# Optimization experiments

Hardware: AMD Instinct MI355X
Metric: run time of the kernel (lower is better)

The kernel has to match this reference:

```python
import jax, jax.numpy as jnp
import numpy as np

N_NODES = 50000
N_EDGES = 400000
LATENT = 128
HIDDEN = 512
N_HEADS = 2          # latent // 64, NodeAttn default num_heads
HEAD_DIM = LATENT // N_HEADS
N_GRAPHS = 500
LN_EPS = 1e-5


def setup_inputs() -> dict:
    key = jax.random.key(0)
    ks = jax.random.split(key, 24)
    s = 0.02
    inp = {
        "edges": jax.random.randint(ks[0], (2, N_EDGES), 0, N_NODES, dtype=jnp.int32),
        "node_feat": jax.random.normal(ks[1], (N_NODES, LATENT), jnp.float32),
        "edge_attr": jax.random.normal(ks[2], (N_EDGES, LATENT), jnp.float32),
        "u": jax.random.normal(ks[3], (N_GRAPHS, LATENT), jnp.float32),
        "num_nodes": jnp.full((N_GRAPHS,), N_NODES // N_GRAPHS, jnp.int32),
        # NodeAttn params (shared for sent/received calls, as in the module)
        "w1": jax.random.normal(ks[4], (3 * LATENT, LATENT), jnp.float32) * s,
        "b1": jnp.zeros((LATENT,), jnp.float32),
        "w2": jax.random.normal(ks[5], (N_HEADS, HEAD_DIM), jnp.float32) * s,
        "w3": jax.random.normal(ks[6], (2 * LATENT, LATENT), jnp.float32) * s,
        "b3": jnp.zeros((LATENT,), jnp.float32),
        # Encoder MLP: 4*latent -> hidden -> hidden -> latent, LN before ReLU
        "mw0": jax.random.normal(ks[7], (4 * LATENT, HIDDEN), jnp.float32) * s,
        "mb0": jnp.zeros((HIDDEN,), jnp.float32),
        "ls0": jnp.ones((HIDDEN,), jnp.float32),
        "lb0": jnp.zeros((HIDDEN,), jnp.float32),
        "mw1": jax.random.normal(ks[8], (HIDDEN, HIDDEN), jnp.float32) * s,
        "mb1": jnp.zeros((HIDDEN,), jnp.float32),
        "ls1": jnp.ones((HIDDEN,), jnp.float32),
        "lb1": jnp.zeros((HIDDEN,), jnp.float32),
        "mw2": jax.random.normal(ks[9], (HIDDEN, LATENT), jnp.float32) * s,
        "mb2": jnp.zeros((LATENT,), jnp.float32),
    }
    return inp


def _layer_norm(x, scale, bias):
    mu = jnp.mean(x, axis=-1, keepdims=True)
    var = jnp.mean(jnp.square(x - mu), axis=-1, keepdims=True)
    return (x - mu) * jax.lax.rsqrt(var + LN_EPS) * scale + bias


def _node_attn(q, k, ea, index, n_nodes, w1, b1, w2, w3, b3):
    # per-edge multi-head scores -> segment softmax over destination index -> scatter-add
    h = jax.nn.leaky_relu(jnp.concatenate([q, k, ea], axis=-1) @ w1 + b1, 0.2)
    h = h.reshape(-1, N_HEADS, HEAD_DIM)                    # [E, H, D]
    logits = jnp.einsum("ehd,hd->eh", h, w2)                 # [E, H]
    m = jax.ops.segment_max(logits, index, num_segments=n_nodes)
    m = jnp.where(jnp.isfinite(m), m, 0.0)                   # empty segments
    e = jnp.exp(logits - m[index])
    z = jax.ops.segment_sum(e, index, num_segments=n_nodes)
    alpha = e / (z[index] + 1e-16)                           # [E, H]
    v = (jnp.concatenate([k, ea], axis=-1) @ w3 + b3).reshape(-1, N_HEADS, HEAD_DIM)
    out = jax.ops.segment_sum(alpha[..., None] * v, index, num_segments=n_nodes)
    return out.reshape(n_nodes, LATENT)


def reference(edges, node_feat, edge_attr, u, num_nodes, w1, b1, w2, w3, b3,
              mw0, mb0, ls0, lb0, mw1, mb1, ls1, lb1, mw2, mb2):
    n = node_feat.shape[0]
    row, col = edges[0], edges[1]
    sent = _node_attn(node_feat[row], node_feat[col], edge_attr, row, n, w1, b1, w2, w3, b3)
    recv = _node_attn(node_feat[col], node_feat[row], edge_attr, col, n, w1, b1, w2, w3, b3)
    glob = jnp.repeat(u, num_nodes, axis=0, total_repeat_length=n)
    x = jnp.concatenate([node_feat, sent, recv, glob], axis=1)   # [N, 4*latent]
    h = jax.nn.relu(_layer_norm(x @ mw0 + mb0, ls0, lb0))
    h = jax.nn.relu(_layer_norm(h @ mw1 + mb1, ls1, lb1))
    return h @ mw2 + mb2
```

## Files before the change

### kernel.cpp

```cpp
#include <hip/hip_runtime.h>
#include <math.h>

#define LATENT 128

typedef __attribute__((ext_vector_type(8))) short bf16x8;
typedef __attribute__((ext_vector_type(4))) float f32x4;
typedef __attribute__((ext_vector_type(2))) float f32x2;
typedef __attribute__((ext_vector_type(2))) unsigned u32x2;
typedef __attribute__((ext_vector_type(4))) unsigned u32x4;

union U4B { uint4 u; bf16x8 v; };

template <typename T>
__device__ __forceinline__ T ntl(const T* p) { return __builtin_nontemporal_load(p); }

__device__ __forceinline__ unsigned short f2bf(float f) {
    unsigned int x = __float_as_uint(f);
    unsigned int r = (x + 0x7fffu + ((x >> 16) & 1u)) >> 16;
    return (unsigned short)r;
}
__device__ __forceinline__ float bf2f(unsigned short h) {
    return __uint_as_float(((unsigned int)h) << 16);
}
__device__ __forceinline__ unsigned pk2(float a, float b) {
    return (unsigned)f2bf(a) | ((unsigned)f2bf(b) << 16);
}
__device__ __forceinline__ float lo16(unsigned u) { return __uint_as_float(u << 16); }
__device__ __forceinline__ float hi16(unsigned u) { return __uint_as_float(u & 0xffff0000u); }

__device__ __forceinline__ void gld16(const void* g, void* l) {
    __builtin_amdgcn_global_load_lds(
        (const __attribute__((address_space(1))) unsigned int*)g,
        (__attribute__((address_space(3))) unsigned int*)l, 16, 0, 0);
}

__global__ void k_gidfill(const int* __restrict__ goff, int G, int n, int* __restrict__ gid) {
    int i = blockIdx.x * 256 + threadIdx.x;
    if (i >= n) return;
    int lo = 0, hi = G - 1;
    while (lo < hi) {
        int mid = (lo + hi + 1) >> 1;
        if (goff[mid] <= i) lo = mid; else hi = mid - 1;
    }
    gid[i] = lo;
}

#define FN  1152
#define FE3 1248
#define FEV 1280
__global__ __launch_bounds__(256) void k_pack2(const float* __restrict__ mw0,
                                               const float* __restrict__ mw1,
                                               const float* __restrict__ mw2,
                                               const float* __restrict__ w1,
                                               const float* __restrict__ w3,
                                               uint4* __restrict__ pw) {
    int tid = blockIdx.x * 256 + threadIdx.x;
    if (tid >= 1312 * 64) return;
    int fid = tid >> 6, lane = tid & 63;
    const float* src; int kt, nt, N;
    if (fid < 512)       { src = mw0;            kt = fid >> 5;           nt = fid & 31;           N = 512; }
    else if (fid < 1024) { src = mw1;            kt = (fid - 512) >> 5;   nt = (fid - 512) & 31;   N = 512; }
    else if (fid < 1152) { src = mw2;            kt = (fid - 1024) >> 3;  nt = (fid - 1024) & 7;   N = 128; }
    else if (fid < 1184) { src = w1;             kt = (fid - 1152) >> 3;  nt = (fid - 1152) & 7;   N = 128; }
    else if (fid < 1216) { src = w1 + 128 * 128; kt = (fid - 1184) >> 3;  nt = (fid - 1184) & 7;   N = 128; }
    else if (fid < 1248) { src = w3;             kt = (fid - 1216) >> 3;  nt = (fid - 1216) & 7;   N = 128; }
    else if (fid < 1280) { src = w1 + 256 * 128; kt = (fid - 1248) >> 3;  nt = (fid - 1248) & 7;   N = 128; }
    else                 { src = w3 + 128 * 128; kt = (fid - 1280) >> 3;  nt = (fid - 1280) & 7;   N = 128; }
    int col = nt * 16 + (lane & 15);
    int k0 = kt * 32 + (lane >> 4) * 8;
    unsigned int w[4];
#pragma unroll
    for (int p = 0; p < 4; ++p) {
        unsigned int lo = f2bf(src[(size_t)(k0 + 2 * p) * N + col]);
        unsigned int hi = f2bf(src[(size_t)(k0 + 2 * p + 1) * N + col]);
        w[p] = lo | (hi << 16);
    }
    pw[(size_t)fid * 64 + lane] = make_uint4(w[0], w[1], w[2], w[3]);
}

__global__ void k_count(const int* __restrict__ edges, int E,
                        int* __restrict__ deg_s, int* __restrict__ deg_r) {
    int e = blockIdx.x * 256 + threadIdx.x;
    if (e < E) { atomicAdd(&deg_s[edges[e]], 1); atomicAdd(&deg_r[edges[E + e]], 1); }
}

__global__ __launch_bounds__(1024) void k_scan(const int* __restrict__ deg, int n,
                                               int* __restrict__ rowptr, int* __restrict__ cursor) {
    __shared__ int wsum[16];
    int t = threadIdx.x;
    int chunk = (n + 1023) / 1024;
    int s = t * chunk; if (s > n) s = n;
    int epos = s + chunk; if (epos > n) epos = n;
    int sum = 0;
    for (int i = s; i < epos; ++i) sum += deg[i];
    int lane = t & 63, wid = t >> 6;
    int v = sum;
#pragma unroll
    for (int d = 1; d < 64; d <<= 1) { int o = __shfl_up(v, d); if (lane >= d) v += o; }
    if (lane == 63) wsum[wid] = v;
    __syncthreads();
    if (t < 16) {
        int wv = wsum[t];
#pragma unroll
        for (int d = 1; d < 16; d <<= 1) { int o = __shfl_up(wv, d, 16); if (t >= d) wv += o; }
        wsum[t] = wv;
    }
    __syncthreads();
    int woff = wid ? wsum[wid - 1] : 0;
    int run = v + woff - sum;
    for (int i = s; i < epos; ++i) { rowptr[i] = run; if (cursor) cursor[i] = run; run += deg[i]; }
    if (t == 1023) rowptr[n] = run;
}

__global__ void k_fill(const int* __restrict__ edges, int E,
                       int* __restrict__ cur_s, int* __restrict__ cur_r,
                       int* __restrict__ sm_s, int* __restrict__ sm_r) {
    int e = blockIdx.x * 256 + threadIdx.x;
    if (e < E) {
        int r = edges[e], c = edges[E + e];
        sm_s[e] = atomicAdd(&cur_s[r], 1);
        sm_r[e] = atomicAdd(&cur_r[c], 1);
    }
}

__global__ __launch_bounds__(512) void k_nodepre2(const float* __restrict__ nf, int n,
                                                  const uint4* __restrict__ pw,
                                                  unsigned short* __restrict__ PQK,
                                                  unsigned short* __restrict__ PVh) {
    __shared__ uint4 xs[32 * 64];
    int t = threadIdx.x, lane = t & 63, w = t >> 6;
    int wr = w >> 2, wc = w & 3, l15 = lane & 15, lg = lane >> 4;
    int base = blockIdx.x * 128;
#pragma unroll
    for (int it = 0; it < 4; ++it) {
        int chunk = t + it * 512;
        int row = chunk >> 4, k8 = chunk & 15, k = k8 * 8;
        int node = base + row;
        f32x4 v0 = (f32x4)(0.f), v1 = (f32x4)(0.f);
        if (node < n) {
            const f32x4* s4 = (const f32x4*)(nf + (size_t)node * 128 + k);
            v0 = ntl(s4); v1 = ntl(s4 + 1);
        }
        uint4 pkv;
        pkv.x = pk2(v0.x, v0.y); pkv.y = pk2(v0.z, v0.w);
        pkv.z = pk2(v1.x, v1.y); pkv.w = pk2(v1.z, v1.w);
        int kt = k >> 5, g = (k >> 3) & 3;
        xs[(kt * 8 + (row >> 4)) * 64 + g * 16 + (row & 15)] = pkv;
    }
    __syncthreads();
    f32x4 acc[4][6];
#pragma unroll
    for (int rt = 0; rt < 4; ++rt)
#pragma unroll
        for (int ct = 0; ct < 6; ++ct) acc[rt][ct] = (f32x4)(0.f);
    for (int kt = 0; kt < 4; ++kt) {
        U4B a[4];
#pragma unroll
        for (int rt = 0; rt < 4; ++rt) a[rt].u = xs[(kt * 8 + wr * 4 + rt) * 64 + lane];
        U4B b[6];
#pragma unroll
        for (int ct = 0; ct < 6; ++ct) {
            int nt = wc * 6 + ct;
            int mat = nt >> 3, ntm = nt & 7;
            b[ct].u = pw[(size_t)(FN + mat * 32 + kt * 8 + ntm) * 64 + lane];
        }
#pragma unroll
        for (int rt = 0; rt < 4; ++rt)
#pragma unroll
            for (int ct = 0; ct < 6; ++ct)
                acc[rt][ct] = __builtin_amdgcn_mfma_f32_16x16x32_bf16(a[rt].v, b[ct].v, acc[rt][ct], 0, 0, 0);
    }
#pragma unroll
    for (int rt = 0; rt < 4; ++rt)
#pragma unroll
        for (int ct = 0; ct < 6; ++ct) {
            int nt = wc * 6 + ct;
#pragma unroll
            for (int reg = 0; reg < 4; ++reg) {
                int node = base + (wr * 4 + rt) * 16 + lg * 4 + reg;
                if (node < n) {
                    unsigned short hv = f2bf(acc[rt][ct][reg]);
                    if (nt < 16) PQK[(size_t)node * 256 + nt * 16 + l15] = hv;
                    else         PVh[(size_t)node * 128 + (nt - 16) * 16 + l15] = hv;
                }
            }
        }
}

__global__ __launch_bounds__(256) void k_eproj1(const int* __restrict__ edges,
                                                const float* __restrict__ ea, int E,
                                                const uint4* __restrict__ pw,
                                                const unsigned short* __restrict__ PQK,
                                                const unsigned short* __restrict__ PVh,
                                                const float* __restrict__ b1,
                                                const float* __restrict__ w2,
                                                const float* __restrict__ b3,
                                                const int* __restrict__ sm_s,
                                                const int* __restrict__ sm_r,
                                                unsigned short* __restrict__ Vs,
                                                unsigned short* __restrict__ Vr,
                                                float* __restrict__ ess2, float* __restrict__ ers2) {
    __shared__ char lds[49152];
    uint4* xs = (uint4*)lds;
    char* ldsE = lds + 16384;
    char* ldsV = lds + 32768;
    int t = threadIdx.x, lane = t & 63, w = t >> 6;
    int wc = w, l15 = lane & 15, lg = lane >> 4;
    int base = blockIdx.x * 64;
#pragma unroll
    for (int it = 0; it < 4; ++it) {
        int chunk = t + it * 256;
        int row = chunk >> 4, k8 = chunk & 15, k = k8 * 8;
        int e = base + row;
        f32x4 v0 = (f32x4)(0.f), v1 = (f32x4)(0.f);
        if (e < E) {
            const f32x4* s4 = (const f32x4*)(ea + (size_t)e * 128 + k);
            v0 = ntl(s4); v1 = ntl(s4 + 1);
        }
        uint4 pkv;
        pkv.x = pk2(v0.x, v0.y); pkv.y = pk2(v0.z, v0.w);
        pkv.z = pk2(v1.x, v1.y); pkv.w = pk2(v1.z, v1.w);
        int kt = k >> 5, g = (k >> 3) & 3;
        xs[(kt * 4 + (row >> 4)) * 64 + g * 16 + (row & 15)] = pkv;
    }
    __syncthreads();
#pragma unroll
    for (int pass = 0; pass < 2; ++pass) {
        f32x4 acc[2][4];
#pragma unroll
        for (int rt2 = 0; rt2 < 2; ++rt2)
#pragma unroll
            for (int ct = 0; ct < 4; ++ct) acc[rt2][ct] = (f32x4)(0.f);
        for (int kt = 0; kt < 4; ++kt) {
            U4B a[2];
#pragma unroll
            for (int rt2 = 0; rt2 < 2; ++rt2)
                a[rt2].u = xs[(kt * 4 + pass * 2 + rt2) * 64 + lane];
            U4B b[4];
            b[0].u = pw[(size_t)(FE3 + kt * 8 + wc * 2 + 0) * 64 + lane];
            b[1].u = pw[(size_t)(FE3 + kt * 8 + wc * 2 + 1) * 64 + lane];
            b[2].u = pw[(size_t)(FEV + kt * 8 + wc * 2 + 0) * 64 + lane];
            b[3].u = pw[(size_t)(FEV + kt * 8 + wc * 2 + 1) * 64 + lane];
#pragma unroll
            for (int rt2 = 0; rt2 < 2; ++rt2)
#pragma unroll
                for (int ct = 0; ct < 4; ++ct)
                    acc[rt2][ct] = __builtin_amdgcn_mfma_f32_16x16x32_bf16(a[rt2].v, b[ct].v, acc[rt2][ct], 0, 0, 0);
        }
#pragma unroll
        for (int rt2 = 0; rt2 < 2; ++rt2)
#pragma unroll
            for (int cc = 0; cc < 2; ++cc) {
                int col = (wc * 2 + cc) * 16 + l15;
                float b1c = b1[col], b3c = b3[col];
#pragma unroll
                for (int reg = 0; reg < 4; ++reg) {
                    int e_loc = (pass * 2 + rt2) * 16 + lg * 4 + reg;
                    int off = (e_loc * 256 + col * 2) ^ ((e_loc & 7) << 4);
                    *(unsigned short*)(ldsE + off) = f2bf(acc[rt2][cc][reg] + b1c);
                    *(unsigned short*)(ldsV + off) = f2bf(acc[rt2][2 + cc][reg] + b3c);
                }
            }
    }
    __syncthreads();
    {
        int e4 = lane >> 4, piece = lane & 15;
#pragma unroll
        for (int i = 0; i < 4; ++i) {
            int e_loc = w * 16 + i * 4 + e4;
            int e = base + e_loc;
            if (e < E) {
                int r = edges[e], c = edges[E + e];
                int off = (e_loc * 256 + piece * 16) ^ ((e_loc & 7) << 4);
                u32x4 vev = *(const u32x4*)(ldsV + off);
                u32x4 pvc = *(const u32x4*)(PVh + (size_t)c * 128 + piece * 8);
                u32x4 pvr = *(const u32x4*)(PVh + (size_t)r * 128 + piece * 8);
                u32x4 vs, vr;
#pragma unroll
                for (int q = 0; q < 4; ++q) {
                    float e0 = lo16(vev[q]);
                    float e1 = hi16(vev[q]);
                    vs[q] = pk2(e0 + lo16(pvc[q]), e1 + hi16(pvc[q]));
                    vr[q] = pk2(e0 + lo16(pvr[q]), e1 + hi16(pvr[q]));
                }
                __builtin_nontemporal_store(vs, (u32x4*)(Vs + (size_t)sm_s[e] * 128 + piece * 8));
                __builtin_nontemporal_store(vr, (u32x4*)(Vr + (size_t)sm_r[e] * 128 + piece * 8));
            }
        }
    }
    int esub = lane >> 3, dg = lane & 7;
    float w2r[16];
    {
        const float4* w4 = (const float4*)(w2 + (dg >> 2) * 64 + (dg & 3) * 16);
#pragma unroll
        for (int q = 0; q < 4; ++q) {
            float4 wv = w4[q];
            w2r[q * 4 + 0] = wv.x; w2r[q * 4 + 1] = wv.y; w2r[q * 4 + 2] = wv.z; w2r[q * 4 + 3] = wv.w;
        }
    }
#pragma unroll
    for (int it = 0; it < 2; ++it) {
        int e_loc = w * 16 + it * 8 + esub;
        int e = base + e_loc;
        if (e >= E) break;
        int r = edges[e], c = edges[E + e];
        const uint4* Aqr = (const uint4*)(PQK + ((size_t)r << 8) + dg * 16);
        const uint4* Akc = (const uint4*)(PQK + ((size_t)c << 8) + 128 + dg * 16);
        const uint4* Aqc = (const uint4*)(PQK + ((size_t)c << 8) + dg * 16);
        const uint4* Akr = (const uint4*)(PQK + ((size_t)r << 8) + 128 + dg * 16);
        float ps = 0.f, pr = 0.f;
#pragma unroll
        for (int half = 0; half < 2; ++half) {
            int off3 = (e_loc * 256 + dg * 32 + half * 16) ^ ((e_loc & 7) << 4);
            uint4 ue3 = *(const uint4*)(ldsE + off3);
            uint4 uqr = Aqr[half], ukc = Akc[half], uqc = Aqc[half], ukr = Akr[half];
            unsigned wqr[4] = {uqr.x, uqr.y, uqr.z, uqr.w};
            unsigned wkc[4] = {ukc.x, ukc.y, ukc.z, ukc.w};
            unsigned wqc[4] = {uqc.x, uqc.y, uqc.z, uqc.w};
            unsigned wkr[4] = {ukr.x, ukr.y, ukr.z, ukr.w};
            unsigned we3[4] = {ue3.x, ue3.y, ue3.z, ue3.w};
#pragma unroll
            for (int q = 0; q < 4; ++q) {
#pragma unroll
                for (int hl = 0; hl < 2; ++hl) {
                    int i = half * 8 + q * 2 + hl;
                    float fqr = hl ? hi16(wqr[q]) : lo16(wqr[q]);
                    float fkc = hl ? hi16(wkc[q]) : lo16(wkc[q]);
                    float fqc = hl ? hi16(wqc[q]) : lo16(wqc[q]);
                    float fkr = hl ? hi16(wkr[q]) : lo16(wkr[q]);
                    float com = hl ? hi16(we3[q]) : lo16(we3[q]);
                    float hs = fqr + fkc + com; hs = hs > 0.f ? hs : 0.2f * hs;
                    float hr = fqc + fkr + com; hr = hr > 0.f ? hr : 0.2f * hr;
                    ps += hs * w2r[i]; pr += hr * w2r[i];
                }
            }
        }
        ps += __shfl_xor(ps, 1); ps += __shfl_xor(ps, 2);
        pr += __shfl_xor(pr, 1); pr += __shfl_xor(pr, 2);
        float Es = expf(ps), Er = expf(pr);
        if (dg == 0) {
            __builtin_nontemporal_store(Es, &ess2[(size_t)sm_s[e] * 2]);
            __builtin_nontemporal_store(Er, &ers2[(size_t)sm_r[e] * 2]);
        } else if (dg == 4) {
            __builtin_nontemporal_store(Es, &ess2[(size_t)sm_s[e] * 2 + 1]);
            __builtin_nontemporal_store(Er, &ers2[(size_t)sm_r[e] * 2 + 1]);
        }
    }
}

__global__ __launch_bounds__(256) void k_aggr(int n,
                                              const int* __restrict__ rps, const int* __restrict__ rpr,
                                              const float* __restrict__ ess2, const float* __restrict__ ers2,
                                              const unsigned short* __restrict__ Vs,
                                              const unsigned short* __restrict__ Vr,
                                              unsigned short* __restrict__ out_sh,
                                              unsigned short* __restrict__ out_rh) {
    int w = threadIdx.x >> 6, lane = threadIdx.x & 63;
    int unit = blockIdx.x * 4 + w;
    if (unit >= 2 * n) return;
    bool sent = unit < n;
    int node = sent ? unit : unit - n;
    const int*      rp = sent ? rps : rpr;
    const float*    ex = sent ? ess2 : ers2;
    const unsigned* V  = (const unsigned*)(sent ? Vs : Vr);
    int s0 = rp[node], s1 = rp[node + 1];
    float z0 = 0.f, z1 = 0.f, acca = 0.f, accb = 0.f;
    int j = s0;
    for (; j + 4 <= s1; j += 4) {
        f32x2 ez[4]; unsigned v[4];
#pragma unroll
        for (int q = 0; q < 4; ++q) ez[q] = ntl((const f32x2*)(ex + 2 * (j + q)));
#pragma unroll
        for (int q = 0; q < 4; ++q) v[q] = ntl(V + (size_t)(j + q) * 64 + lane);
#pragma unroll
        for (int q = 0; q < 4; ++q) {
            z0 += ez[q].x; z1 += ez[q].y;
            float aw = (lane < 32) ? ez[q].x : ez[q].y;
            acca += aw * lo16(v[q]); accb += aw * hi16(v[q]);
        }
    }
    for (; j < s1; ++j) {
        f32x2 ez = ntl((const f32x2*)(ex + 2 * j));
        unsigned v = ntl(V + (size_t)j * 64 + lane);
        z0 += ez.x; z1 += ez.y;
        float aw = (lane < 32) ? ez.x : ez.y;
        acca += aw * lo16(v); accb += aw * hi16(v);
    }
    float zz = (lane < 32) ? z0 : z1;
    float rz = 1.f / (zz + 1e-16f);
    unsigned o = pk2(acca * rz, accb * rz);
    unsigned* outp = (unsigned*)(sent ? out_sh : out_rh);
    outp[(size_t)node * 64 + lane] = o;
}

__global__ __launch_bounds__(512, 4) void k_mlp12(
    const float* __restrict__ nf, const unsigned short* __restrict__ out_sh,
    const unsigned short* __restrict__ out_rh,
    const float* __restrict__ u, const int* __restrict__ gid, int n,
    const uint4* __restrict__ pw,
    const float* __restrict__ mb0, const float* __restrict__ ls0, const float* __restrict__ lb0,
    const float* __restrict__ mb1, const float* __restrict__ ls1, const float* __restrict__ lb1,
    const float* __restrict__ mb2, float* __restrict__ out) {
    extern __shared__ char smem[];
    char* hx = smem;
    char* bb = smem + 32768;
    float2* red = (float2*)(smem + 65536);

    int t = threadIdx.x, lane = t & 63, w = t >> 6;
    int wr = w >> 2, wc = w & 3, l15 = lane & 15, lg = lane >> 4;
    int base = blockIdx.x * 32;

    auto stage32 = [&](int fragbase) {
        const uint4* src = pw + (size_t)fragbase * 64;
#pragma unroll
        for (int q = 0; q < 4; ++q)
            gld16(src + q * 512 + t, bb + ((size_t)q * 512 + t) * 16);
    };
    auto stage8 = [&](int fragbase) {
        const uint4* src = pw + (size_t)fragbase * 64;
        gld16(src + t, bb + (size_t)t * 16);
    };

    stage32(0);
#pragma unroll
    for (int it = 0; it < 8; ++it) {
        int chunk = t + it * 512;
        int row = chunk >> 7, kq = chunk & 127;
        int k = kq * 4;
        int node = base + row;
        u32x2 p = (u32x2)(0u);
        if (node < n) {
            int kk = k & 127;
            if (k < 128) {
                f32x4 v = ntl((const f32x4*)(nf + (size_t)node * 128 + kk));
                p.x = pk2(v.x, v.y); p.y = pk2(v.z, v.w);
            } else if (k < 384) {
                const unsigned short* s = (k < 256 ? out_sh : out_rh) + (size_t)node * 128 + kk;
                p = ntl((const u32x2*)s);
            } else {
                f32x4 v = *(const f32x4*)(u + (size_t)gid[node] * 128 + kk);
                p.x = pk2(v.x, v.y); p.y = pk2(v.z, v.w);
            }
        }
        int addr = (row * 1024 + k * 2) ^ ((row & 7) << 4);
        *(u32x2*)(hx + addr) = p;
    }
    __syncthreads();

    f32x4 acc[8];
#pragma unroll
    for (int layer = 0; layer < 2; ++layer) {
        const float* MB = layer ? mb1 : mb0;
        const float* LS = layer ? ls1 : ls0;
        const float* LB = layer ? lb1 : lb0;
        const int fbase = layer ? 512 : 0;
#pragma unroll
        for (int ct = 0; ct < 8; ++ct) acc[ct] = (f32x4)(0.f);

        for (int kt = 0; kt < 16; ++kt) {
            U4B b[8];
#pragma unroll
            for (int ct = 0; ct < 8; ++ct)
                b[ct].u = *(const uint4*)(bb + (((size_t)wc * 8 + ct) * 64 + lane) * 16);
            U4B a;
            {
                int row = wr * 16 + l15;
                int addr = (row * 1024 + kt * 64 + lg * 16) ^ ((row & 7) << 4);
                a.u = *(const uint4*)(hx + addr);
            }
            __syncthreads();
            if (kt < 15)            stage32(fbase + (kt + 1) * 32);
            else if (layer == 0)    stage32(512);
            else                    stage8(1024);
            __builtin_amdgcn_s_setprio(1);
#pragma unroll
            for (int ct = 0; ct < 8; ++ct)
                acc[ct] = __builtin_amdgcn_mfma_f32_16x16x32_bf16(a.v, b[ct].v, acc[ct], 0, 0, 0);
            __builtin_amdgcn_s_setprio(0);
            __syncthreads();
        }

        float mbv[8], lsv[8], lbv[8];
#pragma unroll
        for (int ct = 0; ct < 8; ++ct) {
            int col = wc * 128 + ct * 16 + l15;
            mbv[ct] = MB[col]; lsv[ct] = LS[col]; lbv[ct] = LB[col];
        }
#pragma unroll
        for (int reg = 0; reg < 4; ++reg) {
            float p = 0.f, q = 0.f;
#pragma unroll
            for (int ct = 0; ct < 8; ++ct) {
                float y = acc[ct][reg] + mbv[ct];
                acc[ct][reg] = y;
                p += y; q += y * y;
            }
#pragma unroll
            for (int d = 1; d < 16; d <<= 1) { p += __shfl_xor(p, d); q += __shfl_xor(q, d); }
            if (l15 == 0) {
                int row = wr * 16 + lg * 4 + reg;
                red[row * 4 + wc] = make_float2(p, q);
            }
        }
        __syncthreads();
#pragma unroll
        for (int reg = 0; reg < 4; ++reg) {
            int row = wr * 16 + lg * 4 + reg;
            float2 r0 = red[row * 4 + 0], r1 = red[row * 4 + 1];
            float2 r2 = red[row * 4 + 2], r3 = red[row * 4 + 3];
            float S = r0.x + r1.x + r2.x + r3.x;
            float S2 = r0.y + r1.y + r2.y + r3.y;
            float mu = S * (1.f / 512.f);
            float var = S2 * (1.f / 512.f) - mu * mu;
            float rs = rsqrtf(var + 1e-5f);
            int rswz = (row & 7) << 4;
#pragma unroll
            for (int ct = 0; ct < 8; ++ct) {
                float h = (acc[ct][reg] - mu) * rs * lsv[ct] + lbv[ct];
                h = fmaxf(h, 0.f);
                int col = wc * 128 + ct * 16 + l15;
                int addr = (row * 1024 + col * 2) ^ rswz;
                *(unsigned short*)(hx + addr) = f2bf(h);
            }
        }
        __syncthreads();
    }

    f32x4 a2[2];
#pragma unroll
    for (int ct = 0; ct < 2; ++ct) a2[ct] = (f32x4)(0.f);
    for (int kt = 0; kt < 16; ++kt) {
        U4B b[2];
#pragma unroll
        for (int ct = 0; ct < 2; ++ct)
            b[ct].u = *(const uint4*)(bb + (((size_t)wc * 2 + ct) * 64 + lane) * 16);
        U4B a;
        {
            int row = wr * 16 + l15;
            int addr = (row * 1024 + kt * 64 + lg * 16) ^ ((row & 7) << 4);
            a.u = *(const uint4*)(hx + addr);
        }
        __syncthreads();
        if (kt < 15) stage8(1024 + (kt + 1) * 8);
        __builtin_amdgcn_s_setprio(1);
#pragma unroll
        for (int ct = 0; ct < 2; ++ct)
            a2[ct] = __builtin_amdgcn_mfma_f32_16x16x32_bf16(a.v, b[ct].v, a2[ct], 0, 0, 0);
        __builtin_amdgcn_s_setprio(0);
        __syncthreads();
    }
    float mb2v[2];
#pragma unroll
    for (int ct = 0; ct < 2; ++ct) mb2v[ct] = mb2[wc * 32 + ct * 16 + l15];
#pragma unroll
    for (int reg = 0; reg < 4; ++reg) {
        int node = base + wr * 16 + lg * 4 + reg;
        if (node < n) {
#pragma unroll
            for (int ct = 0; ct < 2; ++ct)
                __builtin_nontemporal_store(a2[ct][reg] + mb2v[ct],
                    &out[(size_t)node * 128 + wc * 32 + ct * 16 + l15]);
        }
    }
}

extern "C" void kernel_launch(void* const* d_in, const int* in_sizes, int n_in,
                              void* d_out, int out_size, void* d_ws, size_t ws_size,
                              hipStream_t stream) {
    const int*   edges     = (const int*)d_in[0];
    const float* nf        = (const float*)d_in[1];
    const float* ea        = (const float*)d_in[2];
    const float* u         = (const float*)d_in[3];
    const int*   num_nodes = (const int*)d_in[4];
    const float* w1  = (const float*)d_in[5];
    const float* b1  = (const float*)d_in[6];
    const float* w2  = (const float*)d_in[7];
    const float* w3  = (const float*)d_in[8];
    const float* b3  = (const float*)d_in[9];
    const float* mw0 = (const float*)d_in[10];
    const float* mb0 = (const float*)d_in[11];
    const float* ls0 = (const float*)d_in[12];
    const float* lb0 = (const float*)d_in[13];
    const float* mw1 = (const float*)d_in[14];
    const float* mb1 = (const float*)d_in[15];
    const float* ls1 = (const float*)d_in[16];
    const float* lb1 = (const float*)d_in[17];
    const float* mw2 = (const float*)d_in[18];
    const float* mb2 = (const float*)d_in[19];

    int E = in_sizes[0] / 2;
    int n = in_sizes[1] / LATENT;
    int G = in_sizes[4];
    float* out = (float*)d_out;

    char* wsb = (char*)d_ws;
    size_t off = 0;
    auto alloc = [&](size_t bytes) { void* p = (void*)(wsb + off); off += (bytes + 15) & ~(size_t)15; return p; };
    uint4*          pw     = (uint4*)alloc((size_t)1312 * 64 * 16);
    unsigned short* PQK    = (unsigned short*)alloc((size_t)n * 256 * 2);
    unsigned short* PVh    = (unsigned short*)alloc((size_t)n * 128 * 2);
    unsigned short* Vs     = (unsigned short*)alloc((size_t)E * 128 * 2);
    unsigned short* Vr     = (unsigned short*)alloc((size_t)E * 128 * 2);
    float*          ess2   = (float*)alloc((size_t)E * 2 * 4);
    float*          ers2   = (float*)alloc((size_t)E * 2 * 4);
    unsigned short* out_sh = (unsigned short*)alloc((size_t)n * 128 * 2);
    unsigned short* out_rh = (unsigned short*)alloc((size_t)n * 128 * 2);
    int*            gid    = (int*)alloc((size_t)n * 4);
    int*            deg_s  = (int*)alloc((size_t)n * 4);
    int*            deg_r  = (int*)alloc((size_t)n * 4);
    int*            cur_s  = (int*)alloc((size_t)n * 4);
    int*            cur_r  = (int*)alloc((size_t)n * 4);
    int*            rps    = (int*)alloc((size_t)(n + 1) * 4);
    int*            rpr    = (int*)alloc((size_t)(n + 1) * 4);
    int*            sm_s   = (int*)alloc((size_t)E * 4);
    int*            sm_r   = (int*)alloc((size_t)E * 4);
    int*            goff   = (int*)alloc((size_t)(G + 1) * 4);
    int*            gcur   = (int*)alloc((size_t)(G + 1) * 4);

    hipMemsetAsync(deg_s, 0, (size_t)2 * n * 4 + 16, stream);

    hipFuncSetAttribute((const void*)k_mlp12, hipFuncAttributeMaxDynamicSharedMemorySize, 66560);

    k_scan<<<1, 1024, 0, stream>>>(num_nodes, G, goff, gcur);
    k_gidfill<<<(n + 255) / 256, 256, 0, stream>>>(goff, G, n, gid);
    k_pack2<<<(1312 * 64 + 255) / 256, 256, 0, stream>>>(mw0, mw1, mw2, w1, w3, pw);
    k_count<<<(E + 255) / 256, 256, 0, stream>>>(edges, E, deg_s, deg_r);
    k_scan<<<1, 1024, 0, stream>>>(deg_s, n, rps, cur_s);
    k_scan<<<1, 1024, 0, stream>>>(deg_r, n, rpr, cur_r);
    k_fill<<<(E + 255) / 256, 256, 0, stream>>>(edges, E, cur_s, cur_r, sm_s, sm_r);
    k_nodepre2<<<(n + 127) / 128, 512, 0, stream>>>(nf, n, pw, PQK, PVh);
    k_eproj1<<<(E + 63) / 64, 256, 0, stream>>>(edges, ea, E, pw, PQK, PVh, b1, w2, b3,
                                                sm_s, sm_r, Vs, Vr, ess2, ers2);
    k_aggr<<<(2 * n + 3) / 4, 256, 0, stream>>>(n, rps, rpr, ess2, ers2, Vs, Vr, out_sh, out_rh);
    k_mlp12<<<(n + 31) / 32, 512, 66560, stream>>>(nf, out_sh, out_rh, u, gid, n, pw,
                                                   mb0, ls0, lb0, mb1, ls1, lb1, mb2, out);
}
```

Before: 744.9 us.

## Load MLP weight fragments directly from global instead of LDS staging

The node MLP kernel no longer stages packed weight fragments into shared memory through global_load_lds with two block barriers per k-step. Each wave now reads its own B fragments straight from global memory, which should hit L2, and feeds them to the MFMAs. This removes the per-iteration __syncthreads and halves LDS use, so more blocks can be resident per CU. In exchange, every wave issues its own global loads of the weights with more latency exposure and no cross-wave sharing, and the setprio hints are dropped.

```diff
diff --git a/kernel.cpp b/kernel.cpp
--- a/kernel.cpp
+++ b/kernel.cpp
@@ -27,12 +27,6 @@
 }
 __device__ __forceinline__ float lo16(unsigned u) { return __uint_as_float(u << 16); }
 __device__ __forceinline__ float hi16(unsigned u) { return __uint_as_float(u & 0xffff0000u); }
-
-__device__ __forceinline__ void gld16(const void* g, void* l) {
-    __builtin_amdgcn_global_load_lds(
-        (const __attribute__((address_space(1))) unsigned int*)g,
-        (__attribute__((address_space(3))) unsigned int*)l, 16, 0, 0);
-}
 
 __global__ void k_gidfill(const int* __restrict__ goff, int G, int n, int* __restrict__ gid) {
     int i = blockIdx.x * 256 + threadIdx.x;
@@ -393,7 +387,7 @@
     outp[(size_t)node * 64 + lane] = o;
 }
 
-__global__ __launch_bounds__(512, 4) void k_mlp12(
+__global__ __launch_bounds__(512, 4) void k_mlp13(
     const float* __restrict__ nf, const unsigned short* __restrict__ out_sh,
     const unsigned short* __restrict__ out_rh,
     const float* __restrict__ u, const int* __restrict__ gid, int n,
@@ -403,25 +397,12 @@
     const float* __restrict__ mb2, float* __restrict__ out) {
     extern __shared__ char smem[];
     char* hx = smem;
-    char* bb = smem + 32768;
-    float2* red = (float2*)(smem + 65536);
+    float2* red = (float2*)(smem + 32768);
 
     int t = threadIdx.x, lane = t & 63, w = t >> 6;
     int wr = w >> 2, wc = w & 3, l15 = lane & 15, lg = lane >> 4;
     int base = blockIdx.x * 32;
 
-    auto stage32 = [&](int fragbase) {
-        const uint4* src = pw + (size_t)fragbase * 64;
-#pragma unroll
-        for (int q = 0; q < 4; ++q)
-            gld16(src + q * 512 + t, bb + ((size_t)q * 512 + t) * 16);
-    };
-    auto stage8 = [&](int fragbase) {
-        const uint4* src = pw + (size_t)fragbase * 64;
-        gld16(src + t, bb + (size_t)t * 16);
-    };
-
-    stage32(0);
 #pragma unroll
     for (int it = 0; it < 8; ++it) {
         int chunk = t + it * 512;
@@ -453,31 +434,28 @@
         const float* MB = layer ? mb1 : mb0;
         const float* LS = layer ? ls1 : ls0;
         const float* LB = layer ? lb1 : lb0;
-        const int fbase = layer ? 512 : 0;
+        const uint4* PW = pw + ((size_t)(layer ? 512 : 0) + wc * 8) * 64 + lane;
 #pragma unroll
         for (int ct = 0; ct < 8; ++ct) acc[ct] = (f32x4)(0.f);
 
         for (int kt = 0; kt < 16; ++kt) {
-            U4B b[8];
-#pragma unroll
-            for (int ct = 0; ct < 8; ++ct)
-                b[ct].u = *(const uint4*)(bb + (((size_t)wc * 8 + ct) * 64 + lane) * 16);
             U4B a;
             {
                 int row = wr * 16 + l15;
                 int addr = (row * 1024 + kt * 64 + lg * 16) ^ ((row & 7) << 4);
                 a.u = *(const uint4*)(hx + addr);
             }
-            __syncthreads();
-            if (kt < 15)            stage32(fbase + (kt + 1) * 32);
-            else if (layer == 0)    stage32(512);
-            else                    stage8(1024);
-            __builtin_amdgcn_s_setprio(1);
-#pragma unroll
-            for (int ct = 0; ct < 8; ++ct)
-                acc[ct] = __builtin_amdgcn_mfma_f32_16x16x32_bf16(a.v, b[ct].v, acc[ct], 0, 0, 0);
-            __builtin_amdgcn_s_setprio(0);
-            __syncthreads();
+#pragma unroll
+            for (int h = 0; h < 2; ++h) {
+                U4B b[4];
+#pragma unroll
+                for (int ct = 0; ct < 4; ++ct)
+                    b[ct].u = PW[(size_t)(kt * 32 + h * 4 + ct) * 64];
+#pragma unroll
+                for (int ct = 0; ct < 4; ++ct)
+                    acc[h * 4 + ct] = __builtin_amdgcn_mfma_f32_16x16x32_bf16(
+                        a.v, b[ct].v, acc[h * 4 + ct], 0, 0, 0);
+            }
         }
 
         float mbv[8], lsv[8], lbv[8];
@@ -529,25 +507,22 @@
     f32x4 a2[2];
 #pragma unroll
     for (int ct = 0; ct < 2; ++ct) a2[ct] = (f32x4)(0.f);
-    for (int kt = 0; kt < 16; ++kt) {
-        U4B b[2];
-#pragma unroll
-        for (int ct = 0; ct < 2; ++ct)
-            b[ct].u = *(const uint4*)(bb + (((size_t)wc * 2 + ct) * 64 + lane) * 16);
-        U4B a;
-        {
-            int row = wr * 16 + l15;
-            int addr = (row * 1024 + kt * 64 + lg * 16) ^ ((row & 7) << 4);
-            a.u = *(const uint4*)(hx + addr);
-        }
-        __syncthreads();
-        if (kt < 15) stage8(1024 + (kt + 1) * 8);
-        __builtin_amdgcn_s_setprio(1);
-#pragma unroll
-        for (int ct = 0; ct < 2; ++ct)
-            a2[ct] = __builtin_amdgcn_mfma_f32_16x16x32_bf16(a.v, b[ct].v, a2[ct], 0, 0, 0);
-        __builtin_amdgcn_s_setprio(0);
-        __syncthreads();
+    {
+        const uint4* PW2 = pw + ((size_t)1024 + wc * 2) * 64 + lane;
+        for (int kt = 0; kt < 16; ++kt) {
+            U4B a, b[2];
+            {
+                int row = wr * 16 + l15;
+                int addr = (row * 1024 + kt * 64 + lg * 16) ^ ((row & 7) << 4);
+                a.u = *(const uint4*)(hx + addr);
+            }
+#pragma unroll
+            for (int ct = 0; ct < 2; ++ct)
+                b[ct].u = PW2[(size_t)(kt * 8 + ct) * 64];
+#pragma unroll
+            for (int ct = 0; ct < 2; ++ct)
+                a2[ct] = __builtin_amdgcn_mfma_f32_16x16x32_bf16(a.v, b[ct].v, a2[ct], 0, 0, 0);
+        }
     }
     float mb2v[2];
 #pragma unroll
@@ -619,7 +594,7 @@
 
     hipMemsetAsync(deg_s, 0, (size_t)2 * n * 4 + 16, stream);
 
-    hipFuncSetAttribute((const void*)k_mlp12, hipFuncAttributeMaxDynamicSharedMemorySize, 66560);
+    hipFuncSetAttribute((const void*)k_mlp13, hipFuncAttributeMaxDynamicSharedMemorySize, 33792);
 
     k_scan<<<1, 1024, 0, stream>>>(num_nodes, G, goff, gcur);
     k_gidfill<<<(n + 255) / 256, 256, 0, stream>>>(goff, G, n, gid);
@@ -632,6 +607,6 @@
     k_eproj1<<<(E + 63) / 64, 256, 0, stream>>>(edges, ea, E, pw, PQK, PVh, b1, w2, b3,
                                                 sm_s, sm_r, Vs, Vr, ess2, ers2);
     k_aggr<<<(2 * n + 3) / 4, 256, 0, stream>>>(n, rps, rpr, ess2, ers2, Vs, Vr, out_sh, out_rh);
-    k_mlp12<<<(n + 31) / 32, 512, 66560, stream>>>(nf, out_sh, out_rh, u, gid, n, pw,
+    k_mlp13<<<(n + 31) / 32, 512, 33792, stream>>>(nf, out_sh, out_rh, u, gid, n, pw,
                                                    mb0, ls0, lb0, mb1, ls1, lb1, mb2, out);
 }
```

After: 729.5 us, median of 2. 2.1% less time.
